# Performance work log

Measured on AMD Instinct MI355X. Metric: run time of the kernel, lower is better.

The kernel has to match this reference:

```python
import jax, jax.numpy as jnp
import numpy as np

B, S, D, H, Dh, F, L, V = 16, 512, 512, 8, 64, 2048, 6, 32000


def _layer_norm(x, g, b):
    m = x.mean(-1, keepdims=True)
    v = ((x - m) ** 2).mean(-1, keepdims=True)
    return (x - m) / jnp.sqrt(v + 1e-5) * g + b


def setup_inputs() -> dict:
    key = jax.random.key(0)
    ks = jax.random.split(key, 18)
    s = 0.02
    x = jax.random.randint(ks[0], (B, S), 0, V)
    batch_length = jax.random.randint(ks[1], (B,), 0, S)
    embed = (jax.random.normal(ks[2], (V, D)) * s).at[0].set(0.0)  # padding_idx=0 row zeroed
    Wq = jax.random.normal(ks[3], (L, D, H * Dh)) * s
    Wk = jax.random.normal(ks[4], (L, D, H * Dh)) * s
    Wv = jax.random.normal(ks[5], (L, D, H * Dh)) * s
    Wo = jax.random.normal(ks[6], (L, H * Dh, D)) * s
    bo = jnp.zeros((L, D))
    ln1_g = jnp.ones((L, D)); ln1_b = jnp.zeros((L, D))
    W1 = jax.random.normal(ks[7], (L, D, F)) * s
    b1 = jnp.zeros((L, F))
    W2 = jax.random.normal(ks[8], (L, F, D)) * s
    b2 = jnp.zeros((L, D))
    ln2_g = jnp.ones((L, D)); ln2_b = jnp.zeros((L, D))
    return dict(x=x, batch_length=batch_length, embed=embed, Wq=Wq, Wk=Wk, Wv=Wv,
                Wo=Wo, bo=bo, ln1_g=ln1_g, ln1_b=ln1_b, W1=W1, b1=b1, W2=W2,
                b2=b2, ln2_g=ln2_g, ln2_b=ln2_b)


def reference(x, batch_length, embed, Wq, Wk, Wv, Wo, bo, ln1_g, ln1_b,
              W1, b1, W2, b2, ln2_g, ln2_b):
    # sinusoidal positional encoding, exact replication (2.0*i/d with full index i)
    pos = jnp.arange(S, dtype=jnp.float32)[:, None]
    i = jnp.arange(D, dtype=jnp.float32)[None, :]
    ang = pos / jnp.power(10000.0, 2.0 * i / D)
    pe = ang.at[:, 0::2].set(jnp.sin(ang[:, 0::2])).at[:, 1::2].set(jnp.cos(ang[:, 1::2]))
    # per-sample PE truncated at batch_length (rest zero)
    len_mask = (jnp.arange(S)[None, :] < batch_length[:, None]).astype(pe.dtype)
    h = embed[x] + pe[None, :, :] * len_mask[:, :, None]  # [B,S,D]
    # padding mask: True where token==0, expanded to [B,S,S]; torch repeat(H,1,1) -> heads major
    pad = (x == 0)
    pmask = jnp.broadcast_to(pad[:, None, :], (B, S, S))
    mrep = jnp.tile(pmask, (H, 1, 1))  # [H*B, S, S], faithful to torch .repeat
    scale = 1.0 / np.sqrt(Dh).astype(np.float32)
    for l in range(L):
        # faithful .view(B*H, -1, Dh) on [B,S,H*Dh] contiguous memory
        q = (h @ Wq[l]).reshape(B * H, S, Dh)
        k = (h @ Wk[l]).reshape(B * H, S, Dh)
        v = (h @ Wv[l]).reshape(B * H, S, Dh)
        att = jnp.einsum('bqd,bkd->bqk', q, k) * scale  # [B*H,S,S]
        att = jnp.where(mrep, -1e9, att)
        att = jax.nn.softmax(att, axis=2)
        ctx = (att @ v).reshape(B, S, H * Dh)
        o = ctx @ Wo[l] + bo[l]
        h = _layer_norm(h + o, ln1_g[l], ln1_b[l])
        f = jax.nn.relu(h @ W1[l] + b1[l]) @ W2[l] + b2[l]
        h = _layer_norm(h + f, ln2_g[l], ln2_b[l])
    return h
```

## Files before the change

### kernel.cpp

```cpp
#include <hip/hip_runtime.h>
#include <hip/hip_bf16.h>
#include <cmath>

#define B_  16
#define S_  512
#define D_  512
#define F_  2048
#define L_  6
#define MT  8192

typedef __attribute__((ext_vector_type(8))) __bf16 bf16x8;
typedef __attribute__((ext_vector_type(4))) float  f32x4;

__device__ __forceinline__ unsigned short f2bf(float f) {
  return __builtin_bit_cast(unsigned short, __float2bfloat16(f));
}

__device__ __forceinline__ void gload16(const void* g, void* l) {
  __builtin_amdgcn_global_load_lds(
      (const __attribute__((address_space(1))) void*)g,
      (__attribute__((address_space(3))) void*)l, 16, 0, 0);
}

__global__ void embed_pe_kernel(const int* __restrict__ x,
                                const int* __restrict__ blen,
                                const float* __restrict__ emb,
                                float* __restrict__ h,
                                unsigned short* __restrict__ hbf) {
  int bs = blockIdx.x;
  int b = bs >> 9, s = bs & 511;
  int tok = x[bs];
  bool pe = s < blen[b];
  const float* er = emb + (long)tok * D_;
  long rb = (long)bs * D_;
  for (int d = threadIdx.x; d < D_; d += 256) {
    float e = er[d];
    if (pe) {
      float ex = (2.0f * (float)d) / 512.0f;
      float ang = (float)s / powf(10000.0f, ex);
      e += (d & 1) ? cosf(ang) : sinf(ang);
    }
    h[rb + d] = e;
    hbf[rb + d] = f2bf(e);
  }
}

__global__ void mask_build_kernel(const int* __restrict__ x,
                                  unsigned int* __restrict__ mw) {
  int t = threadIdx.x;
  int b = t >> 4, wd = t & 15;
  unsigned int m = 0;
  for (int j = 0; j < 32; j++)
    if (x[b * 512 + wd * 32 + j] == 0) m |= (1u << j);
  mw[b * 16 + wd] = m;
}

__global__ __launch_bounds__(256)
void wconv_kernel(const float* __restrict__ in, unsigned short* __restrict__ out,
                  int K, int N, long inls, long outls) {
  __shared__ float tile[32][33];
  const float* ip = in + (long)blockIdx.z * inls;
  unsigned short* op = out + (long)blockIdx.z * outls;
  int k0 = blockIdx.y * 32, n0 = blockIdx.x * 32;
  int tx = threadIdx.x & 31, ty = threadIdx.x >> 5;
  for (int i = ty; i < 32; i += 8) tile[i][tx] = ip[(long)(k0 + i) * N + n0 + tx];
  __syncthreads();
  for (int i = ty; i < 32; i += 8) op[(long)(n0 + i) * K + k0 + tx] = f2bf(tile[tx][i]);
}

template<int BMv>
__global__ __launch_bounds__(256, 2)
void gemm_bf16(const unsigned short* __restrict__ A,
               const unsigned short* __restrict__ Bt,
               const float* __restrict__ bias,
               float* __restrict__ C, unsigned short* __restrict__ Cbf,
               int M, int N, int K, int relu, int qkv) {
  constexpr int MFR = 4;
  constexpr int NFR = (BMv == 128) ? 4 : 2;
  __shared__ unsigned short Al[BMv * 32];
  __shared__ unsigned short Bl[128 * 32];
  int t = threadIdx.x;
  int lane = t & 63, wid = t >> 6;

  int flat = blockIdx.y * gridDim.x + blockIdx.x;
  int npx = (gridDim.x * gridDim.y) >> 3;
  int w = (flat & 7) * npx + (flat >> 3);
  int bx = w % gridDim.x, by = w / gridDim.x;

  int rbase = by * BMv, cbase = bx * 128;
  int wr = (BMv == 128) ? (wid >> 1) * 64 : 0;
  int wc = (BMv == 128) ? (wid & 1) * 64 : wid * 32;

  f32x4 acc[MFR][NFR];
#pragma unroll
  for (int i = 0; i < MFR; i++)
#pragma unroll
    for (int j = 0; j < NFR; j++) acc[i][j] = (f32x4){0.f, 0.f, 0.f, 0.f};

  int srow = t >> 2;
  int sc = (((t & 3) ^ ((t >> 3) & 3)) << 3);
  const unsigned short* Ag  = A  + (long)(rbase + srow) * K + sc;
  const unsigned short* Ag2 = A  + (long)(rbase + (BMv == 128 ? 64 : 0) + srow) * K + sc;
  const unsigned short* Bg  = Bt + (long)(cbase + srow) * K + sc;
  const unsigned short* Bg2 = Bt + (long)(cbase + 64 + srow) * K + sc;
  unsigned short* Ald  = &Al[t * 8];
  unsigned short* Ald2 = &Al[(BMv == 128 ? 2048 : 0) + t * 8];
  unsigned short* Bld  = &Bl[t * 8];
  unsigned short* Bld2 = &Bl[2048 + t * 8];

  int fr = lane & 15;
  int c4 = lane >> 4;

  for (int kt = 0; kt < K; kt += 32) {
    gload16(Ag + kt, Ald);
    if (BMv == 128) gload16(Ag2 + kt, Ald2);
    gload16(Bg + kt, Bld);
    gload16(Bg2 + kt, Bld2);
    __syncthreads();

    bf16x8 a[MFR], b[NFR];
#pragma unroll
    for (int m = 0; m < MFR; m++) {
      int R = wr + m * 16 + fr;
      a[m] = *(const bf16x8*)&Al[R * 32 + ((c4 ^ ((R >> 1) & 3)) << 3)];
    }
#pragma unroll
    for (int n = 0; n < NFR; n++) {
      int R = wc + n * 16 + fr;
      b[n] = *(const bf16x8*)&Bl[R * 32 + ((c4 ^ ((R >> 1) & 3)) << 3)];
    }
#pragma unroll
    for (int m = 0; m < MFR; m++)
#pragma unroll
      for (int n = 0; n < NFR; n++)
        acc[m][n] = __builtin_amdgcn_mfma_f32_16x16x32_bf16(a[m], b[n], acc[m][n], 0, 0, 0);
    __syncthreads();
  }

  if (BMv == 128 && qkv) {
#pragma unroll
    for (int m = 0; m < MFR; m++) {
#pragma unroll
      for (int n = 0; n < NFR; n++) {
        int col = cbase + wc + n * 16 + fr;
#pragma unroll
        for (int j = 0; j < 4; j++) {
          long row = rbase + wr + m * 16 + (lane >> 4) * 4 + j;
          unsigned short v = f2bf(acc[m][n][j]);
          if (col < 1024) {
            Cbf[(col < 512 ? 0L : 4194304L - 512L) + row * 512 + col] = v;
          } else {
            int cc = col - 1024;
            Cbf[8388608L + (row >> 6) * 32768 + (long)(cc & 63) * 512 +
                ((row & 63) << 3) + (cc >> 6)] = v;
          }
        }
      }
    }
  } else {
#pragma unroll
    for (int m = 0; m < MFR; m++) {
#pragma unroll
      for (int n = 0; n < NFR; n++) {
        int col = cbase + wc + n * 16 + fr;
        float bv = bias ? bias[col] : 0.0f;
#pragma unroll
        for (int j = 0; j < 4; j++) {
          long row = rbase + wr + m * 16 + (lane >> 4) * 4 + j;
          float v = acc[m][n][j] + bv;
          if (relu) v = fmaxf(v, 0.0f);
          if (C)   C[row * N + col] = v;
          if (Cbf) Cbf[row * N + col] = f2bf(v);
        }
      }
    }
  }
}

__global__ __launch_bounds__(256, 2)
void attn_mfma(const unsigned short* __restrict__ qbf,
               const unsigned short* __restrict__ kbf,
               const unsigned short* __restrict__ vtbf,
               const unsigned int* __restrict__ maskw,
               unsigned short* __restrict__ ctxbf) {
  __shared__ unsigned short sb[8192];
  int t = threadIdx.x;
  int lane = t & 63, w = t >> 6;
  int c = lane & 15, h = lane >> 4;

  int flat = blockIdx.y * 8 + blockIdx.x;
  int wk = (flat & 7) * 128 + (flat >> 3);
  int qt = wk & 7, bh = wk >> 3;

  long bhb = (long)bh << 15;
  int mb = bh & 15;

  const uint4* mp = (const uint4*)(maskw + mb * 16);
  uint4 m0 = mp[0], m1 = mp[1], m2 = mp[2], m3 = mp[3];
  unsigned int mwa[16] = {m0.x, m0.y, m0.z, m0.w, m1.x, m1.y, m1.z, m1.w,
                          m2.x, m2.y, m2.z, m2.w, m3.x, m3.y, m3.z, m3.w};

  const bf16x8* qp = (const bf16x8*)(qbf + bhb + (long)(qt * 64 + w * 16 + c) * 64);
  bf16x8 qf0 = qp[h], qf1 = qp[h + 4];

  f32x4 acc[32];
#pragma unroll
  for (int F = 0; F < 32; F++) acc[F] = (f32x4){0.f, 0.f, 0.f, 0.f};

#pragma unroll
  for (int ch = 0; ch < 4; ch++) {
    __syncthreads();
#pragma unroll
    for (int i = 0; i < 4; i++) {
      int idx = t + 256 * i;
      int kr = idx >> 3, g = idx & 7;
      gload16(kbf + bhb + (long)(ch * 128 + kr) * 64 + ((g ^ (kr & 7)) << 3),
              &sb[idx * 8]);
    }
    __syncthreads();
#pragma unroll
    for (int f = 0; f < 8; f++) {
      int R = f * 16 + c;
      int ro = R * 64;
      bf16x8 a0 = *(const bf16x8*)&sb[ro + ((h ^ (R & 7)) << 3)];
      bf16x8 a1 = *(const bf16x8*)&sb[ro + (((h + 4) ^ (R & 7)) << 3)];
      acc[ch * 8 + f] = __builtin_amdgcn_mfma_f32_16x16x32_bf16(a0, qf0, acc[ch * 8 + f], 0, 0, 0);
      acc[ch * 8 + f] = __builtin_amdgcn_mfma_f32_16x16x32_bf16(a1, qf1, acc[ch * 8 + f], 0, 0, 0);
    }
  }

#pragma unroll
  for (int F = 0; F < 32; F++) {
    unsigned int nib = (mwa[F >> 1] >> (((F & 1) << 4) + (h << 2))) & 0xFu;
#pragma unroll
    for (int j = 0; j < 4; j++)
      acc[F][j] = (nib & (1u << j)) ? -1e9f : acc[F][j] * 0.125f;
  }

  float mx = -3.0e38f;
#pragma unroll
  for (int F = 0; F < 32; F++)
#pragma unroll
    for (int j = 0; j < 4; j++) mx = fmaxf(mx, acc[F][j]);
  mx = fmaxf(mx, __shfl_xor(mx, 16));
  mx = fmaxf(mx, __shfl_xor(mx, 32));
  float sm = 0.f;
#pragma unroll
  for (int F = 0; F < 32; F++)
#pragma unroll
    for (int j = 0; j < 4; j++) {
      float e = __expf(acc[F][j] - mx);
      acc[F][j] = e;
      sm += e;
    }
  sm += __shfl_xor(sm, 16);
  sm += __shfl_xor(sm, 32);

  unsigned int pk[64];
#pragma unroll
  for (int F = 0; F < 32; F++) {
    pk[2 * F]     = (unsigned int)f2bf(acc[F][0]) | ((unsigned int)f2bf(acc[F][1]) << 16);
    pk[2 * F + 1] = (unsigned int)f2bf(acc[F][2]) | ((unsigned int)f2bf(acc[F][3]) << 16);
  }

  float rs0 = 1.0f / __shfl(sm, h * 4 + 0);
  float rs1 = 1.0f / __shfl(sm, h * 4 + 1);
  float rs2 = 1.0f / __shfl(sm, h * 4 + 2);
  float rs3 = 1.0f / __shfl(sm, h * 4 + 3);

  f32x4 o[4];
#pragma unroll
  for (int n = 0; n < 4; n++) o[n] = (f32x4){0.f, 0.f, 0.f, 0.f};
  int l0 = c | ((lane & 16) << 1);
  int l1 = l0 + 16;
  bool hb = (lane & 32) != 0;

#pragma unroll
  for (int ch = 0; ch < 4; ch++) {
    __syncthreads();
#pragma unroll
    for (int i = 0; i < 4; i++) {
      int idx = t + 256 * i;
      int d = idx >> 4, g = idx & 15;
      gload16(vtbf + bhb + (long)d * 512 + ch * 128 + ((g ^ (d & 15)) << 3),
              &sb[idx * 8]);
    }
    __syncthreads();
#pragma unroll
    for (int sub = 0; sub < 4; sub++) {
      int kt4 = (ch * 4 + sub) * 4;
      unsigned int a0 = __shfl((int)pk[kt4],     l0);
      unsigned int a1 = __shfl((int)pk[kt4 + 1], l0);
      unsigned int a2 = __shfl((int)pk[kt4],     l1);
      unsigned int a3 = __shfl((int)pk[kt4 + 1], l1);
      unsigned int b0 = __shfl((int)pk[kt4 + 2], l0);
      unsigned int b1 = __shfl((int)pk[kt4 + 3], l0);
      unsigned int b2 = __shfl((int)pk[kt4 + 2], l1);
      unsigned int b3 = __shfl((int)pk[kt4 + 3], l1);
      uint4 aw;
      aw.x = hb ? b0 : a0; aw.y = hb ? b1 : a1;
      aw.z = hb ? b2 : a2; aw.w = hb ? b3 : a3;
      bf16x8 af = __builtin_bit_cast(bf16x8, aw);
#pragma unroll
      for (int n = 0; n < 4; n++) {
        int dl = n * 16 + c;
        bf16x8 vf = *(const bf16x8*)&sb[dl * 128 + (((sub * 4 + h) ^ (dl & 15)) << 3)];
        o[n] = __builtin_amdgcn_mfma_f32_16x16x32_bf16(af, vf, o[n], 0, 0, 0);
      }
    }
  }

  unsigned short* cp = ctxbf + bhb + (long)(qt * 64 + w * 16) * 64;
#pragma unroll
  for (int n = 0; n < 4; n++) {
    cp[(h * 4 + 0) * 64 + n * 16 + c] = f2bf(o[n][0] * rs0);
    cp[(h * 4 + 1) * 64 + n * 16 + c] = f2bf(o[n][1] * rs1);
    cp[(h * 4 + 2) * 64 + n * 16 + c] = f2bf(o[n][2] * rs2);
    cp[(h * 4 + 3) * 64 + n * 16 + c] = f2bf(o[n][3] * rs3);
  }
}

__global__ __launch_bounds__(256)
void ln_kernel(const float* __restrict__ a, const float* __restrict__ r,
               const float* __restrict__ g, const float* __restrict__ be,
               float* __restrict__ out, unsigned short* __restrict__ outbf) {
  int w = threadIdx.x >> 6, lane = threadIdx.x & 63;
  long row = (long)blockIdx.x * 4 + w;
  long base = row * D_ + lane * 8;
  float4 a0 = *(const float4*)(a + base);
  float4 a1 = *(const float4*)(a + base + 4);
  float4 r0 = *(const float4*)(r + base);
  float4 r1 = *(const float4*)(r + base + 4);
  float xv[8] = {a0.x + r0.x, a0.y + r0.y, a0.z + r0.z, a0.w + r0.w,
                 a1.x + r1.x, a1.y + r1.y, a1.z + r1.z, a1.w + r1.w};
  float s = 0;
#pragma unroll
  for (int e = 0; e < 8; e++) s += xv[e];
#pragma unroll
  for (int off = 1; off < 64; off <<= 1) s += __shfl_xor(s, off);
  float m = s * (1.0f / 512.0f);
  float vs = 0;
#pragma unroll
  for (int e = 0; e < 8; e++) { float d = xv[e] - m; vs += d * d; }
#pragma unroll
  for (int off = 1; off < 64; off <<= 1) vs += __shfl_xor(vs, off);
  float rstd = 1.0f / sqrtf(vs * (1.0f / 512.0f) + 1e-5f);
  int gb = lane * 8;
  float o[8];
#pragma unroll
  for (int e = 0; e < 8; e++) o[e] = (xv[e] - m) * rstd * g[gb + e] + be[gb + e];
  *(float4*)(out + base)     = make_float4(o[0], o[1], o[2], o[3]);
  *(float4*)(out + base + 4) = make_float4(o[4], o[5], o[6], o[7]);
  ushort4 u0, u1;
  u0.x = f2bf(o[0]); u0.y = f2bf(o[1]); u0.z = f2bf(o[2]); u0.w = f2bf(o[3]);
  u1.x = f2bf(o[4]); u1.y = f2bf(o[5]); u1.z = f2bf(o[6]); u1.w = f2bf(o[7]);
  *(ushort4*)(outbf + base)     = u0;
  *(ushort4*)(outbf + base + 4) = u1;
}

extern "C" void kernel_launch(void* const* d_in, const int* in_sizes, int n_in,
                              void* d_out, int out_size, void* d_ws, size_t ws_size,
                              hipStream_t stream) {
  const int*   x    = (const int*)d_in[0];
  const int*   blen = (const int*)d_in[1];
  const float* emb  = (const float*)d_in[2];
  const float* Wq   = (const float*)d_in[3];
  const float* Wk   = (const float*)d_in[4];
  const float* Wv   = (const float*)d_in[5];
  const float* Wo   = (const float*)d_in[6];
  const float* bo   = (const float*)d_in[7];
  const float* ln1g = (const float*)d_in[8];
  const float* ln1b = (const float*)d_in[9];
  const float* W1   = (const float*)d_in[10];
  const float* b1   = (const float*)d_in[11];
  const float* W2   = (const float*)d_in[12];
  const float* b2   = (const float*)d_in[13];
  const float* ln2g = (const float*)d_in[14];
  const float* ln2b = (const float*)d_in[15];
  float* out = (float*)d_out;

  float* ws_f = (float*)d_ws;
  const long M4 = 4194304L;
  float* h   = ws_f;
  float* tmp = ws_f + M4;
  unsigned short* U = (unsigned short*)(ws_f + 2 * M4);
  unsigned short* h_bf   = U;
  unsigned short* q_bf   = U + M4;
  unsigned short* k_bf   = U + 2 * M4;
  unsigned short* vt_bf  = U + 3 * M4;
  unsigned short* ctx_bf = U + 4 * M4;
  unsigned short* mid_bf = q_bf;
  unsigned short* Wqkvt  = U + 5 * M4;
  unsigned short* Wot    = Wqkvt + 6L * 1536 * 512;
  unsigned short* W1t    = Wot   + 6L * 512 * 512;
  unsigned short* W2t    = W1t   + 6L * 2048 * 512;
  unsigned int*   maskw  = (unsigned int*)(W2t + 6L * 512 * 2048);

  wconv_kernel<<<dim3(16, 16, 6), 256, 0, stream>>>(Wq, Wqkvt,            512, 512,  262144L, 786432L);
  wconv_kernel<<<dim3(16, 16, 6), 256, 0, stream>>>(Wk, Wqkvt + 262144,   512, 512,  262144L, 786432L);
  wconv_kernel<<<dim3(16, 16, 6), 256, 0, stream>>>(Wv, Wqkvt + 524288,   512, 512,  262144L, 786432L);
  wconv_kernel<<<dim3(16, 16, 6), 256, 0, stream>>>(Wo, Wot,              512, 512,  262144L, 262144L);
  wconv_kernel<<<dim3(64, 16, 6), 256, 0, stream>>>(W1, W1t,              512, 2048, 1048576L, 1048576L);
  wconv_kernel<<<dim3(16, 64, 6), 256, 0, stream>>>(W2, W2t,              2048, 512, 1048576L, 1048576L);
  mask_build_kernel<<<1, 256, 0, stream>>>(x, maskw);
  embed_pe_kernel<<<MT, 256, 0, stream>>>(x, blen, emb, h, h_bf);

  dim3 gqkv(12, 64), g2048(16, 64), g512b(4, 128), gattn(8, 128);

  for (int l = 0; l < L_; l++) {
    const unsigned short* wqkv = Wqkvt + (long)l * 1536 * 512;
    const unsigned short* wo   = Wot   + (long)l * 512 * 512;
    const unsigned short* w1   = W1t   + (long)l * 2048 * 512;
    const unsigned short* w2   = W2t   + (long)l * 512 * 2048;

    gemm_bf16<128><<<gqkv, 256, 0, stream>>>(h_bf, wqkv, nullptr, nullptr, q_bf,
                                             MT, 1536, 512, 0, 1);
    attn_mfma<<<gattn, 256, 0, stream>>>(q_bf, k_bf, vt_bf, maskw, ctx_bf);
    gemm_bf16<64><<<g512b, 256, 0, stream>>>(ctx_bf, wo, bo + (long)l * D_, tmp, nullptr,
                                             MT, 512, 512, 0, 0);
    ln_kernel<<<MT / 4, 256, 0, stream>>>(h, tmp, ln1g + (long)l * D_,
                                          ln1b + (long)l * D_, h, h_bf);
    gemm_bf16<128><<<g2048, 256, 0, stream>>>(h_bf, w1, b1 + (long)l * F_, nullptr, mid_bf,
                                              MT, 2048, 512, 1, 0);
    gemm_bf16<64><<<g512b, 256, 0, stream>>>(mid_bf, w2, b2 + (long)l * D_, tmp, nullptr,
                                             MT, 512, 2048, 0, 0);
    ln_kernel<<<MT / 4, 256, 0, stream>>>(h, tmp, ln2g + (long)l * D_,
                                          ln2b + (long)l * D_,
                                          (l == L_ - 1) ? out : h, h_bf);
  }
}
```

Baseline: 0.9996 ms.

## Double-buffer LDS tiles in GEMM and attention to overlap loads with MFMA

Turns the GEMM K-loop and both attention chunk loops into two-stage pipelines with double-buffered shared memory. The next tile is issued with async global-to-LDS loads before computing the current one, and explicit vmcnt waits plus raw barriers replace __syncthreads. The first V chunk is prefetched during the last K chunk. This hides global load latency behind MFMA work, at the cost of doubled LDS use, which may reduce occupancy. The 64-row GEMM launch-bounds hint is raised to 3 to compensate.

Result: no change. 986.0 us (-1.4%).

```diff
diff --git a/kernel.cpp b/kernel.cpp
--- a/kernel.cpp
+++ b/kernel.cpp
@@ -68,8 +68,8 @@
   for (int i = ty; i < 32; i += 8) op[(long)(n0 + i) * K + k0 + tx] = f2bf(tile[tx][i]);
 }
 
-template<int BMv>
-__global__ __launch_bounds__(256, 2)
+template<int BMv, int MINW>
+__global__ __launch_bounds__(256, MINW)
 void gemm_bf16(const unsigned short* __restrict__ A,
                const unsigned short* __restrict__ Bt,
                const float* __restrict__ bias,
@@ -77,8 +77,8 @@
                int M, int N, int K, int relu, int qkv) {
   constexpr int MFR = 4;
   constexpr int NFR = (BMv == 128) ? 4 : 2;
-  __shared__ unsigned short Al[BMv * 32];
-  __shared__ unsigned short Bl[128 * 32];
+  __shared__ unsigned short Al[2][BMv * 32];
+  __shared__ unsigned short Bl[2][128 * 32];
   int t = threadIdx.x;
   int lane = t & 63, wid = t >> 6;
 
@@ -100,41 +100,53 @@
   int srow = t >> 2;
   int sc = (((t & 3) ^ ((t >> 3) & 3)) << 3);
   const unsigned short* Ag  = A  + (long)(rbase + srow) * K + sc;
-  const unsigned short* Ag2 = A  + (long)(rbase + (BMv == 128 ? 64 : 0) + srow) * K + sc;
+  const unsigned short* Ag2 = A  + (long)(rbase + 64 + srow) * K + sc;
   const unsigned short* Bg  = Bt + (long)(cbase + srow) * K + sc;
   const unsigned short* Bg2 = Bt + (long)(cbase + 64 + srow) * K + sc;
-  unsigned short* Ald  = &Al[t * 8];
-  unsigned short* Ald2 = &Al[(BMv == 128 ? 2048 : 0) + t * 8];
-  unsigned short* Bld  = &Bl[t * 8];
-  unsigned short* Bld2 = &Bl[2048 + t * 8];
+
+  auto stage = [&](int bi, int kt) {
+    gload16(Ag + kt, &Al[bi][t * 8]);
+    if constexpr (BMv == 128) gload16(Ag2 + kt, &Al[bi][2048 + t * 8]);
+    gload16(Bg + kt, &Bl[bi][t * 8]);
+    gload16(Bg2 + kt, &Bl[bi][2048 + t * 8]);
+  };
 
   int fr = lane & 15;
   int c4 = lane >> 4;
 
-  for (int kt = 0; kt < K; kt += 32) {
-    gload16(Ag + kt, Ald);
-    if (BMv == 128) gload16(Ag2 + kt, Ald2);
-    gload16(Bg + kt, Bld);
-    gload16(Bg2 + kt, Bld2);
-    __syncthreads();
+  int nt = K >> 5;
+  stage(0, 0);
+  int cur = 0;
+  for (int tt = 0; tt < nt; ++tt) {
+    if (tt + 1 < nt) {
+      stage(cur ^ 1, (tt + 1) << 5);
+      if constexpr (BMv == 128)
+        asm volatile("s_waitcnt vmcnt(4)" ::: "memory");
+      else
+        asm volatile("s_waitcnt vmcnt(3)" ::: "memory");
+    } else {
+      asm volatile("s_waitcnt vmcnt(0)" ::: "memory");
+    }
+    __builtin_amdgcn_s_barrier();
 
     bf16x8 a[MFR], b[NFR];
 #pragma unroll
     for (int m = 0; m < MFR; m++) {
       int R = wr + m * 16 + fr;
-      a[m] = *(const bf16x8*)&Al[R * 32 + ((c4 ^ ((R >> 1) & 3)) << 3)];
+      a[m] = *(const bf16x8*)&Al[cur][R * 32 + ((c4 ^ ((R >> 1) & 3)) << 3)];
     }
 #pragma unroll
     for (int n = 0; n < NFR; n++) {
       int R = wc + n * 16 + fr;
-      b[n] = *(const bf16x8*)&Bl[R * 32 + ((c4 ^ ((R >> 1) & 3)) << 3)];
+      b[n] = *(const bf16x8*)&Bl[cur][R * 32 + ((c4 ^ ((R >> 1) & 3)) << 3)];
     }
 #pragma unroll
     for (int m = 0; m < MFR; m++)
 #pragma unroll
       for (int n = 0; n < NFR; n++)
         acc[m][n] = __builtin_amdgcn_mfma_f32_16x16x32_bf16(a[m], b[n], acc[m][n], 0, 0, 0);
-    __syncthreads();
+    __builtin_amdgcn_s_barrier();
+    cur ^= 1;
   }
 
   if (BMv == 128 && qkv) {
@@ -183,7 +195,7 @@
                const unsigned short* __restrict__ vtbf,
                const unsigned int* __restrict__ maskw,
                unsigned short* __restrict__ ctxbf) {
-  __shared__ unsigned short sb[8192];
+  __shared__ unsigned short sb[2][8192];
   int t = threadIdx.x;
   int lane = t & 63, w = t >> 6;
   int c = lane & 15, h = lane >> 4;
@@ -203,30 +215,48 @@
   const bf16x8* qp = (const bf16x8*)(qbf + bhb + (long)(qt * 64 + w * 16 + c) * 64);
   bf16x8 qf0 = qp[h], qf1 = qp[h + 4];
 
-  f32x4 acc[32];
-#pragma unroll
-  for (int F = 0; F < 32; F++) acc[F] = (f32x4){0.f, 0.f, 0.f, 0.f};
-
-#pragma unroll
-  for (int ch = 0; ch < 4; ch++) {
-    __syncthreads();
+  auto stageK = [&](int bi, int ch) {
 #pragma unroll
     for (int i = 0; i < 4; i++) {
       int idx = t + 256 * i;
       int kr = idx >> 3, g = idx & 7;
       gload16(kbf + bhb + (long)(ch * 128 + kr) * 64 + ((g ^ (kr & 7)) << 3),
-              &sb[idx * 8]);
-    }
-    __syncthreads();
+              &sb[bi][idx * 8]);
+    }
+  };
+  auto stageV = [&](int bi, int ch) {
+#pragma unroll
+    for (int i = 0; i < 4; i++) {
+      int idx = t + 256 * i;
+      int d = idx >> 4, g = idx & 15;
+      gload16(vtbf + bhb + (long)d * 512 + ch * 128 + ((g ^ (d & 15)) << 3),
+              &sb[bi][idx * 8]);
+    }
+  };
+
+  f32x4 acc[32];
+#pragma unroll
+  for (int F = 0; F < 32; F++) acc[F] = (f32x4){0.f, 0.f, 0.f, 0.f};
+
+  stageK(0, 0);
+  int cur = 0;
+#pragma unroll
+  for (int ch = 0; ch < 4; ch++) {
+    if (ch < 3) stageK(cur ^ 1, ch + 1);
+    else        stageV(cur ^ 1, 0);
+    asm volatile("s_waitcnt vmcnt(4)" ::: "memory");
+    __builtin_amdgcn_s_barrier();
 #pragma unroll
     for (int f = 0; f < 8; f++) {
       int R = f * 16 + c;
       int ro = R * 64;
-      bf16x8 a0 = *(const bf16x8*)&sb[ro + ((h ^ (R & 7)) << 3)];
-      bf16x8 a1 = *(const bf16x8*)&sb[ro + (((h + 4) ^ (R & 7)) << 3)];
+      bf16x8 a0 = *(const bf16x8*)&sb[cur][ro + ((h ^ (R & 7)) << 3)];
+      bf16x8 a1 = *(const bf16x8*)&sb[cur][ro + (((h + 4) ^ (R & 7)) << 3)];
       acc[ch * 8 + f] = __builtin_amdgcn_mfma_f32_16x16x32_bf16(a0, qf0, acc[ch * 8 + f], 0, 0, 0);
       acc[ch * 8 + f] = __builtin_amdgcn_mfma_f32_16x16x32_bf16(a1, qf1, acc[ch * 8 + f], 0, 0, 0);
     }
+    __builtin_amdgcn_s_barrier();
+    cur ^= 1;
   }
 
 #pragma unroll
@@ -277,15 +307,13 @@
 
 #pragma unroll
   for (int ch = 0; ch < 4; ch++) {
-    __syncthreads();
-#pragma unroll
-    for (int i = 0; i < 4; i++) {
-      int idx = t + 256 * i;
-      int d = idx >> 4, g = idx & 15;
-      gload16(vtbf + bhb + (long)d * 512 + ch * 128 + ((g ^ (d & 15)) << 3),
-              &sb[idx * 8]);
-    }
-    __syncthreads();
+    if (ch < 3) {
+      stageV(cur ^ 1, ch + 1);
+      asm volatile("s_waitcnt vmcnt(4)" ::: "memory");
+    } else {
+      asm volatile("s_waitcnt vmcnt(0)" ::: "memory");
+    }
+    __builtin_amdgcn_s_barrier();
 #pragma unroll
     for (int sub = 0; sub < 4; sub++) {
       int kt4 = (ch * 4 + sub) * 4;
@@ -304,10 +332,12 @@
 #pragma unroll
       for (int n = 0; n < 4; n++) {
         int dl = n * 16 + c;
-        bf16x8 vf = *(const bf16x8*)&sb[dl * 128 + (((sub * 4 + h) ^ (dl & 15)) << 3)];
+        bf16x8 vf = *(const bf16x8*)&sb[cur][dl * 128 + (((sub * 4 + h) ^ (dl & 15)) << 3)];
         o[n] = __builtin_amdgcn_mfma_f32_16x16x32_bf16(af, vf, o[n], 0, 0, 0);
       }
     }
+    __builtin_amdgcn_s_barrier();
+    cur ^= 1;
   }
 
   unsigned short* cp = ctxbf + bhb + (long)(qt * 64 + w * 16) * 64;
@@ -413,17 +443,17 @@
     const unsigned short* w1   = W1t   + (long)l * 2048 * 512;
     const unsigned short* w2   = W2t   + (long)l * 512 * 2048;
 
-    gemm_bf16<128><<<gqkv, 256, 0, stream>>>(h_bf, wqkv, nullptr, nullptr, q_bf,
-                                             MT, 1536, 512, 0, 1);
+    gemm_bf16<128, 2><<<gqkv, 256, 0, stream>>>(h_bf, wqkv, nullptr, nullptr, q_bf,
+                                                MT, 1536, 512, 0, 1);
     attn_mfma<<<gattn, 256, 0, stream>>>(q_bf, k_bf, vt_bf, maskw, ctx_bf);
-    gemm_bf16<64><<<g512b, 256, 0, stream>>>(ctx_bf, wo, bo + (long)l * D_, tmp, nullptr,
-                                             MT, 512, 512, 0, 0);
+    gemm_bf16<64, 3><<<g512b, 256, 0, stream>>>(ctx_bf, wo, bo + (long)l * D_, tmp, nullptr,
+                                                MT, 512, 512, 0, 0);
     ln_kernel<<<MT / 4, 256, 0, stream>>>(h, tmp, ln1g + (long)l * D_,
                                           ln1b + (long)l * D_, h, h_bf);
-    gemm_bf16<128><<<g2048, 256, 0, stream>>>(h_bf, w1, b1 + (long)l * F_, nullptr, mid_bf,
-                                              MT, 2048, 512, 1, 0);
-    gemm_bf16<64><<<g512b, 256, 0, stream>>>(mid_bf, w2, b2 + (long)l * D_, tmp, nullptr,
-                                             MT, 512, 2048, 0, 0);
+    gemm_bf16<128, 2><<<g2048, 256, 0, stream>>>(h_bf, w1, b1 + (long)l * F_, nullptr, mid_bf,
+                                                 MT, 2048, 512, 1, 0);
+    gemm_bf16<64, 3><<<g512b, 256, 0, stream>>>(mid_bf, w2, b2 + (long)l * D_, tmp, nullptr,
+                                                MT, 512, 2048, 0, 0);
     ln_kernel<<<MT / 4, 256, 0, stream>>>(h, tmp, ln2g + (long)l * D_,
                                           ln2b + (long)l * D_,
                                           (l == L_ - 1) ? out : h, h_bf);
```
